# Optimization experiments

Hardware: AMD Instinct MI355X
Metric: run time of the kernel (lower is better)

## Reference

```python
import jax, jax.numpy as jnp
import numpy as np

N_EMBED = 1024
N_HEADS = 16
HEAD_DIM = N_EMBED // N_HEADS


def setup_inputs() -> dict:
    key = jax.random.key(0)
    ks = jax.random.split(key, 5)
    B, T, C = 4, 2048, N_EMBED
    s_in = 1.0 / np.sqrt(C)
    x = jax.random.normal(ks[0], (B, T, C), dtype=jnp.float32)
    W_qkv = jax.random.normal(ks[1], (C, 3 * C), dtype=jnp.float32) * s_in
    b_qkv = jnp.zeros((3 * C,), dtype=jnp.float32)
    W_out = jax.random.normal(ks[2], (C, C), dtype=jnp.float32) * s_in
    b_out = jnp.zeros((C,), dtype=jnp.float32)
    return {"x": x, "W_qkv": W_qkv, "b_qkv": b_qkv, "W_out": W_out, "b_out": b_out}


def reference(x, W_qkv, b_qkv, W_out, b_out):
    B, T, C = x.shape
    H, D = N_HEADS, HEAD_DIM
    qkv = x @ W_qkv + b_qkv                       # [B,T,3C]
    q, k, v = jnp.split(qkv, 3, axis=-1)
    # [B,T,C] -> [B,H,T,D]
    q = q.reshape(B, T, H, D).transpose(0, 2, 1, 3)
    k = k.reshape(B, T, H, D).transpose(0, 2, 1, 3)
    v = v.reshape(B, T, H, D).transpose(0, 2, 1, 3)
    scale = 1.0 / np.sqrt(D)
    attn = jnp.einsum('bhqd,bhkd->bhqk', q, k) * scale   # [B,H,T,T]
    causal = jnp.tril(jnp.ones((T, T), dtype=bool))
    attn = jnp.where(causal, attn, -jnp.inf)
    attn = jax.nn.softmax(attn, axis=-1)
    out = jnp.einsum('bhqk,bhkd->bhqd', attn, v)          # [B,H,T,D]
    out = out.transpose(0, 2, 1, 3).reshape(B, T, C)
    return out @ W_out + b_out
```

## Files before the change

### kernel.cpp

```cpp
#include <hip/hip_runtime.h>
#include <stdint.h>

#define BB 4
#define TT 2048
#define CC 1024
#define HH 16
#define DD 64
#define MM (BB*TT)

typedef __bf16 bf16x8 __attribute__((ext_vector_type(8)));
typedef float  f32x4  __attribute__((ext_vector_type(4)));

__device__ __forceinline__ unsigned short f2bf(float f) {
  __bf16 h = (__bf16)f;
  union { __bf16 h; unsigned short u; } c; c.h = h;
  return c.u;
}

__device__ __forceinline__ void glds16(const void* g, void* l) {
  __builtin_amdgcn_global_load_lds((const __attribute__((address_space(1))) void*)g,
                                   (__attribute__((address_space(3))) void*)l,
                                   16, 0, 0);
}

__device__ __forceinline__ void perm32swap(uint32_t& a, uint32_t& b) {
  asm volatile("v_permlane32_swap_b32 %0, %1" : "+v"(a), "+v"(b));
}
__device__ __forceinline__ void perm16swap(uint32_t& a, uint32_t& b) {
  asm volatile("v_permlane16_swap_b32 %0, %1" : "+v"(a), "+v"(b));
}

__device__ __forceinline__ int xcd_swz(int bid, int nwg) {
  if (nwg & 7) return bid;
  return (bid & 7) * (nwg >> 3) + (bid >> 3);
}

typedef unsigned short u16x8 __attribute__((ext_vector_type(8)));
__global__ void f32_to_bf16_kn(const float* __restrict__ in,
                               unsigned short* __restrict__ out, int n) {
  int i = (blockIdx.x * blockDim.x + threadIdx.x) * 8;
  const int stride = gridDim.x * blockDim.x * 8;
  for (; i < n; i += stride) {
    float4 a = *(const float4*)&in[i];
    float4 b = *(const float4*)&in[i + 4];
    u16x8 t;
    t[0]=f2bf(a.x); t[1]=f2bf(a.y); t[2]=f2bf(a.z); t[3]=f2bf(a.w);
    t[4]=f2bf(b.x); t[5]=f2bf(b.y); t[6]=f2bf(b.z); t[7]=f2bf(b.w);
    *(u16x8*)&out[i] = t;
  }
}

__global__ void transpose_to_bf16(const float* __restrict__ in,
                                  unsigned short* __restrict__ out,
                                  int R, int Cc) {
  __shared__ float tile[32][33];
  const int c0 = blockIdx.x * 32, r0 = blockIdx.y * 32;
  const int tx = threadIdx.x & 31, ty = threadIdx.x >> 5;
#pragma unroll
  for (int i = 0; i < 32; i += 8)
    tile[ty + i][tx] = in[(size_t)(r0 + ty + i) * Cc + c0 + tx];
  __syncthreads();
#pragma unroll
  for (int i = 0; i < 32; i += 8)
    out[(size_t)(c0 + ty + i) * R + r0 + tx] = f2bf(tile[tx][ty + i]);
}

template<int MODE>
__global__ void gemm128(const unsigned short* __restrict__ A,
                        const unsigned short* __restrict__ Bt,
                        const float* __restrict__ bias,
                        void* __restrict__ outp,
                        int M, int N, int K)
{
  __shared__ unsigned short Alds[128 * 32];
  __shared__ unsigned short Blds[128 * 32];
  const int tid = threadIdx.x;
  const int lane = tid & 63;
  const int wid  = tid >> 6;
  const int wm = wid >> 1, wn = wid & 1;
  const int nwg = (int)(gridDim.x * gridDim.y);
  const int swz = xcd_swz((int)(blockIdx.y * gridDim.x + blockIdx.x), nwg);
  const int m0 = (swz / (int)gridDim.x) * 128;
  const int n0 = (swz % (int)gridDim.x) * 128;
  const int l15 = lane & 15, l4 = lane >> 4;

  f32x4 acc[4][4];
#pragma unroll
  for (int i = 0; i < 4; i++)
#pragma unroll
    for (int j = 0; j < 4; j++) acc[i][j] = (f32x4){0.f, 0.f, 0.f, 0.f};

  for (int k0 = 0; k0 < K; k0 += 32) {
    __syncthreads();
#pragma unroll
    for (int c = 0; c < 2; ++c) {
      const int chunk = wid * 2 + c;
      const int linear = chunk * 1024 + lane * 16;
      const int row  = linear >> 6;
      const int colb = linear & 63;
      glds16((const char*)A  + ((size_t)(m0 + row) * K + k0) * 2 + colb,
             (char*)Alds + chunk * 1024);
      glds16((const char*)Bt + ((size_t)(n0 + row) * K + k0) * 2 + colb,
             (char*)Blds + chunk * 1024);
    }
    __syncthreads();
    bf16x8 af[4], bfr[4];
#pragma unroll
    for (int i = 0; i < 4; i++)
      af[i]  = *(const bf16x8*)&Alds[(wm * 64 + i * 16 + l15) * 32 + l4 * 8];
#pragma unroll
    for (int j = 0; j < 4; j++)
      bfr[j] = *(const bf16x8*)&Blds[(wn * 64 + j * 16 + l15) * 32 + l4 * 8];
#pragma unroll
    for (int i = 0; i < 4; i++)
#pragma unroll
      for (int j = 0; j < 4; j++)
        acc[i][j] = __builtin_amdgcn_mfma_f32_16x16x32_bf16(af[i], bfr[j], acc[i][j], 0, 0, 0);
  }

#pragma unroll
  for (int i = 0; i < 4; i++) {
#pragma unroll
    for (int j = 0; j < 4; j++) {
      const int n = n0 + wn * 64 + j * 16 + l15;
      const float bn = bias[n];
#pragma unroll
      for (int r = 0; r < 4; r++) {
        const int m = m0 + wm * 64 + i * 16 + l4 * 4 + r;
        float v = acc[i][j][r] + bn;
        if (MODE == 0) {
          unsigned short* qb = (unsigned short*)outp;
          const int which = n >> 10;
          const int cc = n & 1023;
          const int h = cc >> 6, d = cc & 63;
          const int b = m >> 11, t = m & 2047;
          if (which == 0) {
            const size_t off = (((size_t)(b * HH + h)) * TT + t) * DD + d;
            qb[off] = f2bf(v * 0.125f);
          } else if (which == 1) {
            const size_t off = (((size_t)(b * HH + h)) * TT + t) * DD + d;
            qb[(size_t)MM * CC + off] = f2bf(v);
          } else {
            const size_t offv = (((size_t)(b * HH + h)) * DD + d) * TT + t;
            qb[(size_t)2 * MM * CC + offv] = f2bf(v);
          }
        } else {
          float* O = (float*)outp;
          O[(size_t)m * N + n] = v;
        }
      }
    }
  }
}

__global__ void attn_fwd(const unsigned short* __restrict__ qbuf,
                         const unsigned short* __restrict__ kbuf,
                         const unsigned short* __restrict__ vtbuf,
                         unsigned short* __restrict__ ao)
{
  __shared__ unsigned short Klds[2][64 * 64];
  __shared__ unsigned short Vt[2][64 * 64];
  const int tid = threadIdx.x, lane = tid & 63, w = tid >> 6;
  const int l15 = lane & 15, l4 = lane >> 4;
  const int NQT = TT / 64;
  const int nwg = NQT * BB * HH;
  const int swz = xcd_swz((int)blockIdx.x, nwg);
  const int bh = swz / NQT;
  const int qtile = NQT - 1 - (swz % NQT);
  const int q0 = qtile * 64;
  const unsigned short* Qb  = qbuf  + (size_t)bh * TT * DD;
  const unsigned short* Kb  = kbuf  + (size_t)bh * TT * DD;
  const unsigned short* VTb = vtbuf + (size_t)bh * DD * TT;

  const int srow = lane >> 3;
  const int scol = ((lane & 7) ^ srow) * 8;

  bf16x8 qf[2];
#pragma unroll
  for (int ks = 0; ks < 2; ks++)
    qf[ks] = *(const bf16x8*)&Qb[(size_t)(q0 + w * 16 + l15) * DD + ks * 32 + l4 * 8];

  f32x4 o[4];
#pragma unroll
  for (int df = 0; df < 4; df++) o[df] = (f32x4){0.f, 0.f, 0.f, 0.f};
  float m_st = -__builtin_huge_valf();
  float l_st = 0.f;

  const int qwmin = q0 + w * 16;
  const int qrow  = qwmin + l15;
  const int nt = qtile + 1;

#pragma unroll
  for (int j = 0; j < 2; j++) {
    const int g = w * 2 + j;
    const int row = g * 8 + srow;
    glds16(Kb + (size_t)row * DD + scol,       (char*)&Klds[0][0] + g * 1024);
    glds16(VTb + (size_t)row * TT + scol,      (char*)&Vt[0][0]   + g * 1024);
  }

  for (int t = 0; t < nt; t++) {
    __syncthreads();
    if (t + 1 < nt) {
      const int kv1 = (t + 1) * 64;
      const int nb = (t + 1) & 1;
#pragma unroll
      for (int j = 0; j < 2; j++) {
        const int g = w * 2 + j;
        const int row = g * 8 + srow;
        glds16(Kb + (size_t)(kv1 + row) * DD + scol, (char*)&Klds[nb][0] + g * 1024);
        glds16(VTb + (size_t)row * TT + kv1 + scol,  (char*)&Vt[nb][0]   + g * 1024);
      }
    }
    const int cb = t & 1;
    const int kv0 = t * 64;

    if (kv0 <= qwmin + 15) {
      f32x4 s[4];
      __builtin_amdgcn_s_setprio(1);
#pragma unroll
      for (int fc = 0; fc < 4; fc++) {
        s[fc] = (f32x4){0.f, 0.f, 0.f, 0.f};
        const int kr = fc * 16 + l15;
#pragma unroll
        for (int ks = 0; ks < 2; ks++) {
          bf16x8 kf = *(const bf16x8*)&Klds[cb][(kr * 64 + ks * 32 + l4 * 8) ^ ((kr & 7) << 3)];
          s[fc] = __builtin_amdgcn_mfma_f32_16x16x32_bf16(kf, qf[ks], s[fc], 0, 0, 0);
        }
      }
      __builtin_amdgcn_s_setprio(0);
      if (kv0 + 63 > qwmin) {
#pragma unroll
        for (int fc = 0; fc < 4; fc++)
#pragma unroll
          for (int r = 0; r < 4; r++)
            if (kv0 + fc * 16 + l4 * 4 + r > qrow) s[fc][r] = -__builtin_huge_valf();
      }
      float tm = s[0][0];
#pragma unroll
      for (int fc = 0; fc < 4; fc++)
#pragma unroll
        for (int r = 0; r < 4; r++) tm = fmaxf(tm, s[fc][r]);
      tm = fmaxf(tm, __shfl_xor(tm, 16));
      tm = fmaxf(tm, __shfl_xor(tm, 32));
      const float mn = fmaxf(m_st, tm);
      const float sc = __expf(m_st - mn);
      m_st = mn;
      float rs = 0.f;
      uint32_t wpk[4][2];
#pragma unroll
      for (int fc = 0; fc < 4; fc++) {
        float p0 = __expf(s[fc][0] - mn), p1 = __expf(s[fc][1] - mn);
        float p2 = __expf(s[fc][2] - mn), p3 = __expf(s[fc][3] - mn);
        rs += (p0 + p1) + (p2 + p3);
        union { unsigned short u[2]; uint32_t d; } a, b;
        a.u[0] = f2bf(p0); a.u[1] = f2bf(p1);
        b.u[0] = f2bf(p2); b.u[1] = f2bf(p3);
        wpk[fc][0] = a.d; wpk[fc][1] = b.d;
      }
      rs += __shfl_xor(rs, 16);
      rs += __shfl_xor(rs, 32);
      l_st = l_st * sc + rs;
#pragma unroll
      for (int df = 0; df < 4; df++)
#pragma unroll
        for (int r = 0; r < 4; r++) o[df][r] *= sc;
      bf16x8 pa[2];
#pragma unroll
      for (int ks = 0; ks < 2; ks++) {
        uint32_t Aq = wpk[2 * ks][0], Bq = wpk[2 * ks][1];
        uint32_t Cq = wpk[2 * ks + 1][0], Dq = wpk[2 * ks + 1][1];
        perm32swap(Aq, Cq); perm16swap(Aq, Cq);
        perm32swap(Bq, Dq); perm16swap(Bq, Dq);
        union { uint32_t d[4]; bf16x8 v; } pf;
        pf.d[0] = Aq; pf.d[1] = Bq; pf.d[2] = Cq; pf.d[3] = Dq;
        pa[ks] = pf.v;
      }
      __builtin_amdgcn_s_setprio(1);
#pragma unroll
      for (int df = 0; df < 4; df++) {
        const int d = df * 16 + l15;
#pragma unroll
        for (int ks = 0; ks < 2; ks++) {
          bf16x8 vf = *(const bf16x8*)&Vt[cb][(d * 64 + ks * 32 + l4 * 8) ^ ((d & 7) << 3)];
          o[df] = __builtin_amdgcn_mfma_f32_16x16x32_bf16(vf, pa[ks], o[df], 0, 0, 0);
        }
      }
      __builtin_amdgcn_s_setprio(0);
    }
  }

  const int b = bh >> 4, h = bh & 15;
  const float inv = 1.0f / l_st;
#pragma unroll
  for (int df = 0; df < 4; df++)
#pragma unroll
    for (int r = 0; r < 4; r++) {
      const int d = df * 16 + l4 * 4 + r;
      ao[((size_t)(b * TT + qrow)) * CC + h * DD + d] = f2bf(o[df][r] * inv);
    }
}

extern "C" void kernel_launch(void* const* d_in, const int* in_sizes, int n_in,
                              void* d_out, int out_size, void* d_ws, size_t ws_size,
                              hipStream_t stream) {
  const float* x    = (const float*)d_in[0];
  const float* Wqkv = (const float*)d_in[1];
  const float* bqkv = (const float*)d_in[2];
  const float* Wout = (const float*)d_in[3];
  const float* bout = (const float*)d_in[4];
  float* out = (float*)d_out;
  char* ws = (char*)d_ws;

  unsigned short* xb    = (unsigned short*)ws;
  unsigned short* wqkvt = (unsigned short*)(ws + 16777216);
  unsigned short* woutt = (unsigned short*)(ws + 23068672);
  unsigned short* qkv   = (unsigned short*)(ws + 25165824);
  unsigned short* ao    = xb;

  f32_to_bf16_kn<<<2048, 256, 0, stream>>>(x, xb, MM * CC);
  transpose_to_bf16<<<dim3(3 * CC / 32, CC / 32), 256, 0, stream>>>(Wqkv, wqkvt, CC, 3 * CC);
  transpose_to_bf16<<<dim3(CC / 32, CC / 32), 256, 0, stream>>>(Wout, woutt, CC, CC);

  gemm128<0><<<dim3(3 * CC / 128, MM / 128), 256, 0, stream>>>(
      xb, wqkvt, bqkv, (void*)qkv, MM, 3 * CC, CC);

  attn_fwd<<<(TT / 64) * BB * HH, 256, 0, stream>>>(
      qkv, qkv + (size_t)MM * CC, qkv + (size_t)2 * MM * CC, ao);

  gemm128<1><<<dim3(CC / 128, MM / 128), 256, 0, stream>>>(
      ao, woutt, bout, (void*)out, MM, CC, CC);
}
```

Before: 297.6 us.

## Double-buffer GEMM LDS tiles with prefetch and MFMA-fragment-ordered layout

The GEMM kernel now uses two LDS buffers. The next K-tile is fetched with global_load_lds while MFMAs run on the current one, which removes one barrier per iteration. The global load addressing is rearranged so each 1 KB chunk is stored in MFMA fragment order, so each lane reads a contiguous 16-byte fragment without bank conflicts. The MFMA block is wrapped in s_setprio to favor math issue. The cost is double the LDS footprint, and correctness relies on the async LDS writes completing before the single barrier.

```diff
diff --git a/kernel.cpp b/kernel.cpp
--- a/kernel.cpp
+++ b/kernel.cpp
@@ -72,8 +72,8 @@
                         void* __restrict__ outp,
                         int M, int N, int K)
 {
-  __shared__ unsigned short Alds[128 * 32];
-  __shared__ unsigned short Blds[128 * 32];
+  __shared__ unsigned short Alds[2][128 * 32];
+  __shared__ unsigned short Blds[2][128 * 32];
   const int tid = threadIdx.x;
   const int lane = tid & 63;
   const int wid  = tid >> 6;
@@ -84,38 +84,50 @@
   const int n0 = (swz % (int)gridDim.x) * 128;
   const int l15 = lane & 15, l4 = lane >> 4;
 
+  const size_t soffA = (size_t)(m0 + l15) * K + l4 * 8;
+  const size_t soffB = (size_t)(n0 + l15) * K + l4 * 8;
+
   f32x4 acc[4][4];
 #pragma unroll
   for (int i = 0; i < 4; i++)
 #pragma unroll
     for (int j = 0; j < 4; j++) acc[i][j] = (f32x4){0.f, 0.f, 0.f, 0.f};
 
-  for (int k0 = 0; k0 < K; k0 += 32) {
+#pragma unroll
+  for (int c2 = 0; c2 < 2; c2++) {
+    const int c = wid * 2 + c2;
+    glds16(A  + soffA + (size_t)c * 16 * K, (char*)&Alds[0][0] + c * 1024);
+    glds16(Bt + soffB + (size_t)c * 16 * K, (char*)&Blds[0][0] + c * 1024);
+  }
+
+  const int NT = K >> 5;
+  for (int t = 0; t < NT; t++) {
     __syncthreads();
-#pragma unroll
-    for (int c = 0; c < 2; ++c) {
-      const int chunk = wid * 2 + c;
-      const int linear = chunk * 1024 + lane * 16;
-      const int row  = linear >> 6;
-      const int colb = linear & 63;
-      glds16((const char*)A  + ((size_t)(m0 + row) * K + k0) * 2 + colb,
-             (char*)Alds + chunk * 1024);
-      glds16((const char*)Bt + ((size_t)(n0 + row) * K + k0) * 2 + colb,
-             (char*)Blds + chunk * 1024);
-    }
-    __syncthreads();
+    if (t + 1 < NT) {
+      const int nb = (t + 1) & 1;
+      const int k1 = (t + 1) * 32;
+#pragma unroll
+      for (int c2 = 0; c2 < 2; c2++) {
+        const int c = wid * 2 + c2;
+        glds16(A  + soffA + (size_t)c * 16 * K + k1, (char*)&Alds[nb][0] + c * 1024);
+        glds16(Bt + soffB + (size_t)c * 16 * K + k1, (char*)&Blds[nb][0] + c * 1024);
+      }
+    }
+    const int cb = t & 1;
     bf16x8 af[4], bfr[4];
 #pragma unroll
     for (int i = 0; i < 4; i++)
-      af[i]  = *(const bf16x8*)&Alds[(wm * 64 + i * 16 + l15) * 32 + l4 * 8];
+      af[i]  = *(const bf16x8*)&Alds[cb][(wm * 4 + i) * 512 + lane * 8];
 #pragma unroll
     for (int j = 0; j < 4; j++)
-      bfr[j] = *(const bf16x8*)&Blds[(wn * 64 + j * 16 + l15) * 32 + l4 * 8];
+      bfr[j] = *(const bf16x8*)&Blds[cb][(wn * 4 + j) * 512 + lane * 8];
+    __builtin_amdgcn_s_setprio(1);
 #pragma unroll
     for (int i = 0; i < 4; i++)
 #pragma unroll
       for (int j = 0; j < 4; j++)
         acc[i][j] = __builtin_amdgcn_mfma_f32_16x16x32_bf16(af[i], bfr[j], acc[i][j], 0, 0, 0);
+    __builtin_amdgcn_s_setprio(0);
   }
 
 #pragma unroll
```

New measurement: 342.7 us. 1.15x slower.
